# Kernel optimization log

Measured on AMD Instinct MI355X. Metric: run time of the kernel, lower is better.

Reference implementation:

```python
import jax, jax.numpy as jnp
import numpy as np

N_NODES = 100000
N_EDGES = 320000
N_GRAPHS = 4096
HID = 256
NUM_FEAT = 28


def setup_inputs() -> dict:
    key = jax.random.key(0)
    ks = jax.random.split(key, 20)
    inp = {}
    inp['x'] = jax.random.normal(ks[0], (N_NODES, NUM_FEAT), dtype=jnp.float32)
    inp['edge_index'] = jax.random.randint(ks[1], (2, N_EDGES), 0, N_NODES, dtype=jnp.int64)
    inp['batch'] = jnp.sort(jax.random.randint(ks[2], (N_NODES,), 0, N_GRAPHS, dtype=jnp.int64))
    def lin(k, out_d, in_d, scale=None):
        s = scale if scale is not None else 1.0 / np.sqrt(in_d)
        return jax.random.uniform(k, (out_d, in_d), jnp.float32, -s, s)
    # GraphConv layer l: W_rel (neighbor aggregate), b_rel, W_root (self)
    dims = [(HID, NUM_FEAT), (HID, HID), (HID, HID), (HID, HID)]
    for i, (o, d) in enumerate(dims, 1):
        inp[f'W{i}_rel'] = lin(ks[2 + 3 * i], o, d)
        inp[f'b{i}_rel'] = jnp.zeros((o,), jnp.float32)
        inp[f'W{i}_root'] = lin(ks[3 + 3 * i], o, d)
    inp['fc1_w'] = lin(ks[15], HID, 4 * HID)
    inp['fc1_b'] = jnp.zeros((HID,), jnp.float32)
    inp['fc2_w'] = lin(ks[16], HID, HID)
    inp['fc2_b'] = jnp.zeros((HID,), jnp.float32)
    inp['fc3_w'] = lin(ks[17], HID, HID)
    inp['fc3_b'] = jnp.zeros((HID,), jnp.float32)
    inp['fc4_w'] = lin(ks[18], 1, HID)
    inp['fc4_b'] = jnp.zeros((1,), jnp.float32)
    return inp


def _graph_conv(x, src, dst, W_rel, b_rel, W_root):
    # PyG GraphConv (aggr='add'): out = lin_rel(sum_{j->i} x_j) + lin_root(x_i)
    agg = jax.ops.segment_sum(x[src], dst, num_segments=N_NODES)  # [N, d]
    return agg @ W_rel.T + b_rel + x @ W_root.T


def reference(x, edge_index, batch,
              W1_rel, b1_rel, W1_root, W2_rel, b2_rel, W2_root,
              W3_rel, b3_rel, W3_root, W4_rel, b4_rel, W4_root,
              fc1_w, fc1_b, fc2_w, fc2_b, fc3_w, fc3_b, fc4_w, fc4_b):
    src, dst = edge_index[0], edge_index[1]
    x1 = jax.nn.relu(_graph_conv(x, src, dst, W1_rel, b1_rel, W1_root))
    x2 = jax.nn.relu(_graph_conv(x1, src, dst, W2_rel, b2_rel, W2_root))
    x3 = jax.nn.relu(_graph_conv(x2, src, dst, W3_rel, b3_rel, W3_root))
    x4 = jax.nn.relu(_graph_conv(x3, src, dst, W4_rel, b4_rel, W4_root))
    h = jnp.concatenate([x1, x2, x3, x4], axis=-1)  # [N, 4*HID]
    # global mean pool over graphs
    sums = jax.ops.segment_sum(h, batch, num_segments=N_GRAPHS)  # [G, 4*HID]
    cnts = jax.ops.segment_sum(jnp.ones((h.shape[0],), h.dtype), batch, num_segments=N_GRAPHS)
    g = sums / jnp.maximum(cnts, 1.0)[:, None]
    g = jax.nn.relu(g @ fc1_w.T + fc1_b)
    g = jax.nn.relu(g @ fc2_w.T + fc2_b)
    g = jax.nn.relu(g @ fc3_w.T + fc3_b)
    out = g @ fc4_w.T + fc4_b  # [G, 1]
    return out.reshape(-1)
```

## Files before the change

kernel.cpp:

```cpp
#include <hip/hip_runtime.h>
#include <hip/hip_bf16.h>
#include <cstdio>

#define HID 256

using short8  = __attribute__((ext_vector_type(8))) short;
using floatx4 = __attribute__((ext_vector_type(4))) float;

__device__ inline unsigned short bf16_rn(float x) {
    unsigned u = __float_as_uint(x);
    return (unsigned short)((u + 0x7FFFu + ((u >> 16) & 1u)) >> 16);
}

__global__ void marker_k(float* __restrict__ out, int n, float v) {
    int i = blockIdx.x * blockDim.x + threadIdx.x;
    if (i < n) out[i] = v;
}

__global__ void detect64_k(const unsigned* __restrict__ eiw, int E,
                           const unsigned* __restrict__ bw, int Nh,
                           int* __restrict__ any_nonzero) {
    int total = E + Nh;
    unsigned loc = 0;
    for (int i = blockIdx.x * blockDim.x + threadIdx.x; i < total;
         i += gridDim.x * blockDim.x) {
        loc |= (i < E) ? eiw[2 * i + 1] : bw[2 * (i - E) + 1];
    }
    if (loc) atomicOr(any_nonzero, 1);
}

__global__ void norm_idx_k(const int* __restrict__ src, int* __restrict__ dst,
                           int n, const int* __restrict__ any_nonzero) {
    int is64 = (any_nonzero[0] == 0);
    for (int i = blockIdx.x * blockDim.x + threadIdx.x; i < n;
         i += gridDim.x * blockDim.x) {
        dst[i] = is64 ? src[2 * i] : src[i];
    }
}

__global__ void pool_bounds_k(const int* __restrict__ batch, int N, int G,
                              int* __restrict__ starts) {
    int g = blockIdx.x * blockDim.x + threadIdx.x;
    if (g > G) return;
    int lo = 0, hi = N;
    while (lo < hi) {
        int mid = (lo + hi) >> 1;
        if (batch[mid] < g) lo = mid + 1; else hi = mid;
    }
    starts[g] = lo;
}

__global__ void deg_count_k(const int* __restrict__ ei, int E, int N,
                            int* __restrict__ deg) {
    int e = blockIdx.x * blockDim.x + threadIdx.x;
    if (e >= E) return;
    int s = ei[e];
    int d = ei[E + e];
    if ((unsigned)s >= (unsigned)N || (unsigned)d >= (unsigned)N) return;
    atomicAdd(&deg[d], 1);
}

#define SCAN_BLK 256

__global__ __launch_bounds__(SCAN_BLK) void scan_a_k(const int* __restrict__ deg,
                                                     int* __restrict__ bsum, int N) {
    __shared__ int red[SCAN_BLK];
    int i = blockIdx.x * SCAN_BLK + threadIdx.x;
    int v = (i < N) ? deg[i] : 0;
    red[threadIdx.x] = v;
    __syncthreads();
#pragma unroll
    for (int off = SCAN_BLK / 2; off > 0; off >>= 1) {
        if (threadIdx.x < off) red[threadIdx.x] += red[threadIdx.x + off];
        __syncthreads();
    }
    if (threadIdx.x == 0) bsum[blockIdx.x] = red[0];
}

__global__ __launch_bounds__(1024) void scan_b_k(int* __restrict__ bsum, int nb) {
    __shared__ int tsum[1024];
    int t = threadIdx.x;
    int v = (t < nb) ? bsum[t] : 0;
    tsum[t] = v;
    __syncthreads();
    for (int off = 1; off < 1024; off <<= 1) {
        int u = (t >= off) ? tsum[t - off] : 0;
        __syncthreads();
        tsum[t] += u;
        __syncthreads();
    }
    if (t < nb) bsum[t] = tsum[t] - v;
}

__global__ __launch_bounds__(SCAN_BLK) void scan_c_k(const int* __restrict__ deg,
                                                     const int* __restrict__ bsum,
                                                     int* __restrict__ row_ptr, int N) {
    __shared__ int tsum[SCAN_BLK];
    int t = threadIdx.x;
    int i = blockIdx.x * SCAN_BLK + t;
    int v = (i < N) ? deg[i] : 0;
    tsum[t] = v;
    __syncthreads();
    for (int off = 1; off < SCAN_BLK; off <<= 1) {
        int u = (t >= off) ? tsum[t - off] : 0;
        __syncthreads();
        tsum[t] += u;
        __syncthreads();
    }
    if (i <= N) row_ptr[i] = tsum[t] - v + bsum[blockIdx.x];
}

__global__ __launch_bounds__(1024) void scan_rowptr_k(const int* __restrict__ deg,
                                                      int* __restrict__ row_ptr, int N) {
    __shared__ int tsum[1024];
    int t = threadIdx.x;
    int chunk = (N + 1023) / 1024;
    int lo = t * chunk;
    int hi = min(lo + chunk, N);
    int s = 0;
    for (int i = lo; i < hi; i++) s += deg[i];
    tsum[t] = s;
    __syncthreads();
    for (int off = 1; off < 1024; off <<= 1) {
        int v = (t >= off) ? tsum[t - off] : 0;
        __syncthreads();
        tsum[t] += v;
        __syncthreads();
    }
    int run = (t == 0) ? 0 : tsum[t - 1];
    for (int i = lo; i < hi; i++) { row_ptr[i] = run; run += deg[i]; }
    if (hi >= N && lo <= N) row_ptr[N] = run;
}

__global__ void fill_csr_k(const int* __restrict__ ei, int E, int N,
                           const int* __restrict__ row_ptr, int* __restrict__ cursor,
                           int* __restrict__ esrc) {
    int e = blockIdx.x * blockDim.x + threadIdx.x;
    if (e >= E) return;
    int s = ei[e];
    int d = ei[E + e];
    if ((unsigned)s >= (unsigned)N || (unsigned)d >= (unsigned)N) return;
    int pos = atomicAdd(&cursor[d], 1);
    esrc[row_ptr[d] + pos] = s;
}

__global__ void gather28_k(const float* __restrict__ x, const int* __restrict__ row_ptr,
                           const int* __restrict__ esrc, float* __restrict__ Q28, int N) {
    int gid = blockIdx.x * blockDim.x + threadIdx.x;
    int node = gid >> 5;
    if (node >= N) return;
    int lane = gid & 31;
    if (lane >= 28) return;
    int s = row_ptr[node], e = row_ptr[node + 1];
    float acc = 0.f;
    for (int i = s; i < e; i++) {
        int src = esrc[i];
        acc += x[(size_t)src * 28 + lane];
    }
    Q28[(size_t)node * 28 + lane] = acc;
}

__global__ void gather256_k(const float* __restrict__ P, const int* __restrict__ row_ptr,
                            const int* __restrict__ esrc, float* __restrict__ Q, int N) {
    int gid = blockIdx.x * blockDim.x + threadIdx.x;
    int node = gid >> 6;
    if (node >= N) return;
    int lane = gid & 63;
    int s = row_ptr[node], e = row_ptr[node + 1];
    float4 acc = make_float4(0.f, 0.f, 0.f, 0.f);
    for (int i = s; i < e; i++) {
        int src = esrc[i];
        float4 v = *(const float4*)(P + (size_t)src * HID + lane * 4);
        acc.x += v.x; acc.y += v.y; acc.z += v.z; acc.w += v.w;
    }
    *(float4*)(Q + (size_t)node * HID + lane * 4) = acc;
}

__global__ __launch_bounds__(256) void l1_fused_k(
    const float* __restrict__ x, const float* __restrict__ agg,
    const float* __restrict__ Wrel, const float* __restrict__ Wroot,
    const float* __restrict__ bias, float* __restrict__ out, int M) {
    __shared__ float As[64][28];
    __shared__ float Xs[64][28];
    int t = threadIdx.x;
    int n0 = blockIdx.x * 64;
    float wrel[28], wroot[28];
#pragma unroll
    for (int k = 0; k < 28; k++) {
        wrel[k]  = Wrel[t * 28 + k];
        wroot[k] = Wroot[t * 28 + k];
    }
    float b = bias[t];
    for (int idx = t; idx < 64 * 28; idx += 256) {
        int r = idx / 28;
        int c = idx - r * 28;
        int gr = n0 + r;
        As[r][c] = (gr < M) ? agg[(size_t)gr * 28 + c] : 0.f;
        Xs[r][c] = (gr < M) ? x[(size_t)gr * 28 + c] : 0.f;
    }
    __syncthreads();
    int nmax = min(64, M - n0);
    for (int n = 0; n < nmax; n++) {
        float acc = b;
#pragma unroll
        for (int k4 = 0; k4 < 28; k4 += 4) {
            float4 a  = *(const float4*)&As[n][k4];
            float4 xx = *(const float4*)&Xs[n][k4];
            acc += a.x * wrel[k4] + a.y * wrel[k4 + 1] + a.z * wrel[k4 + 2] + a.w * wrel[k4 + 3];
            acc += xx.x * wroot[k4] + xx.y * wroot[k4 + 1] + xx.z * wroot[k4 + 2] + xx.w * wroot[k4 + 3];
        }
        out[(size_t)(n0 + n) * HID + t] = fmaxf(acc, 0.f);
    }
}

__global__ void wsplit6_k(const float* W0, const float* W1, const float* W2,
                          const float* W3, const float* W4, const float* W5,
                          unsigned short* __restrict__ out_hl, int n) {
    int i = blockIdx.x * blockDim.x + threadIdx.x;
    if (i >= n) return;
    const float* W = (blockIdx.y == 0) ? W0 : (blockIdx.y == 1) ? W1 :
                     (blockIdx.y == 2) ? W2 : (blockIdx.y == 3) ? W3 :
                     (blockIdx.y == 4) ? W4 : W5;
    unsigned short* o = out_hl + (size_t)blockIdx.y * 2 * n;
    float a = W[i];
    unsigned short h = bf16_rn(a);
    float hf = __uint_as_float(((unsigned)h) << 16);
    o[i] = h;
    o[n + i] = bf16_rn(a - hf);
}

#define LSTR 40

__global__ __launch_bounds__(256) void gemm_strip_mfma_k(
    const float* __restrict__ Q, const unsigned short* __restrict__ Wr_hl,
    float* __restrict__ P, const unsigned short* __restrict__ Wo_hl,
    const float* __restrict__ bias, int M) {
    __shared__ unsigned short Ah[64 * LSTR], Al[64 * LSTR];
    __shared__ unsigned short Wh[256 * LSTR], Wl[256 * LSTR];
    int t = threadIdx.x;
    int brow = blockIdx.x * 64;
    int w = t >> 6;
    int l = t & 63;

    floatx4 acc[4][4];
#pragma unroll
    for (int i = 0; i < 4; i++)
#pragma unroll
        for (int j = 0; j < 4; j++) acc[i][j] = (floatx4){0.f, 0.f, 0.f, 0.f};

    int srow = t >> 2;
    int sg   = t & 3;

    for (int ch = 0; ch < 16; ch++) {
        int phase2 = (ch >= 8);
        const float* A = phase2 ? P : Q;
        const unsigned short* Whl = phase2 ? Wo_hl : Wr_hl;
        int kbase = (ch & 7) * 32;

        {
            int gr = brow + srow;
            float v[8];
            if (gr < M) {
                float4 u0 = *(const float4*)(A + (size_t)gr * HID + kbase + sg * 8);
                float4 u1 = *(const float4*)(A + (size_t)gr * HID + kbase + sg * 8 + 4);
                v[0] = u0.x; v[1] = u0.y; v[2] = u0.z; v[3] = u0.w;
                v[4] = u1.x; v[5] = u1.y; v[6] = u1.z; v[7] = u1.w;
            } else {
#pragma unroll
                for (int j = 0; j < 8; j++) v[j] = 0.f;
            }
            union { unsigned short us[8]; short8 v8; } hh, ll;
#pragma unroll
            for (int j = 0; j < 8; j++) {
                unsigned short h = bf16_rn(v[j]);
                float hf = __uint_as_float(((unsigned)h) << 16);
                hh.us[j] = h;
                ll.us[j] = bf16_rn(v[j] - hf);
            }
            int base = srow * LSTR + sg * 8;
            *(short8*)(Ah + base) = hh.v8;
            *(short8*)(Al + base) = ll.v8;
        }
#pragma unroll
        for (int i = 0; i < 4; i++) {
            int col = srow + i * 64;
            short8 hh = *(const short8*)(Whl + (size_t)col * HID + kbase + sg * 8);
            short8 ll = *(const short8*)(Whl + 65536 + (size_t)col * HID + kbase + sg * 8);
            int base = col * LSTR + sg * 8;
            *(short8*)(Wh + base) = hh;
            *(short8*)(Wl + base) = ll;
        }
        __syncthreads();

        int frow = l & 15;
        int fg   = l >> 4;
        short8 ahf[4], alf[4], whf[4], wlf[4];
#pragma unroll
        for (int rt = 0; rt < 4; rt++) {
            int base = (rt * 16 + frow) * LSTR + fg * 8;
            ahf[rt] = *(short8*)(Ah + base);
            alf[rt] = *(short8*)(Al + base);
        }
#pragma unroll
        for (int ct = 0; ct < 4; ct++) {
            int base = (w * 64 + ct * 16 + frow) * LSTR + fg * 8;
            whf[ct] = *(short8*)(Wh + base);
            wlf[ct] = *(short8*)(Wl + base);
        }
#pragma unroll
        for (int rt = 0; rt < 4; rt++)
#pragma unroll
            for (int ct = 0; ct < 4; ct++) {
                acc[rt][ct] = __builtin_amdgcn_mfma_f32_16x16x32_bf16(
                    ahf[rt], whf[ct], acc[rt][ct], 0, 0, 0);
                acc[rt][ct] = __builtin_amdgcn_mfma_f32_16x16x32_bf16(
                    alf[rt], whf[ct], acc[rt][ct], 0, 0, 0);
                acc[rt][ct] = __builtin_amdgcn_mfma_f32_16x16x32_bf16(
                    ahf[rt], wlf[ct], acc[rt][ct], 0, 0, 0);
            }
        __syncthreads();
    }

#pragma unroll
    for (int ct = 0; ct < 4; ct++) {
        int gc = w * 64 + ct * 16 + (l & 15);
        float bs = bias[gc];
#pragma unroll
        for (int rt = 0; rt < 4; rt++) {
            floatx4 a = acc[rt][ct];
#pragma unroll
            for (int r = 0; r < 4; r++) {
                int gr = brow + rt * 16 + (l >> 4) * 4 + r;
                if (gr < M)
                    P[(size_t)gr * HID + gc] = fmaxf(a[r] + bs, 0.f);
            }
        }
    }
}

#define BM 64
#define BN 64
#define BK 32
#define LP 68

__global__ __launch_bounds__(256) void gemm_dual_k(
    const float* __restrict__ A1, int lda1, const float* __restrict__ W1,
    const float* __restrict__ A2, int lda2, const float* __restrict__ W2,
    const float* __restrict__ bias, float* __restrict__ out, int ldout,
    int M, int K1, int K2, int relu) {
    __shared__ float As[BK][LP];
    __shared__ float Ws[BK][LP];
    int t = threadIdx.x;
    int brow = blockIdx.x * BM;
    int bcol = blockIdx.y * BN;
    int tx = t & 15, ty = t >> 4;
    float acc[4][4] = {{0.f}};
    int Ktot = K1 + K2;
    int srow = t >> 3;
    int sk4 = (t & 7) << 2;

    for (int kk = 0; kk < Ktot; kk += BK) {
        int phase2 = (kk >= K1);
        const float* A = phase2 ? A2 : A1;
        const float* W = phase2 ? W2 : W1;
        int lda = phase2 ? lda2 : lda1;
        int ldw = phase2 ? K2 : K1;
        int kbase = phase2 ? (kk - K1) : kk;
#pragma unroll
        for (int i = 0; i < 2; i++) {
            int r = srow + i * 32;
            int gr = brow + r;
            float4 v = make_float4(0.f, 0.f, 0.f, 0.f);
            if (gr < M) v = *(const float4*)(A + (size_t)gr * lda + kbase + sk4);
            As[sk4 + 0][r] = v.x; As[sk4 + 1][r] = v.y;
            As[sk4 + 2][r] = v.z; As[sk4 + 3][r] = v.w;
            float4 w = *(const float4*)(W + (size_t)(bcol + r) * ldw + kbase + sk4);
            Ws[sk4 + 0][r] = w.x; Ws[sk4 + 1][r] = w.y;
            Ws[sk4 + 2][r] = w.z; Ws[sk4 + 3][r] = w.w;
        }
        __syncthreads();
#pragma unroll
        for (int k = 0; k < BK; k++) {
            float4 a = *(const float4*)&As[k][ty << 2];
            float4 w = *(const float4*)&Ws[k][tx << 2];
            float av[4] = {a.x, a.y, a.z, a.w};
            float wv[4] = {w.x, w.y, w.z, w.w};
#pragma unroll
            for (int i = 0; i < 4; i++)
#pragma unroll
                for (int j = 0; j < 4; j++)
                    acc[i][j] = fmaf(av[i], wv[j], acc[i][j]);
        }
        __syncthreads();
    }
#pragma unroll
    for (int i = 0; i < 4; i++) {
        int gr = brow + (ty << 2) + i;
        if (gr >= M) continue;
#pragma unroll
        for (int j = 0; j < 4; j++) {
            int gc = bcol + (tx << 2) + j;
            float v = acc[i][j] + bias[gc];
            if (relu) v = fmaxf(v, 0.f);
            out[(size_t)gr * ldout + gc] = v;
        }
    }
}

__global__ __launch_bounds__(256) void pool_slice_k(const float* __restrict__ xl,
                                                    const int* __restrict__ starts,
                                                    float* __restrict__ gslice, int N) {
    int g = blockIdx.x;
    int t = threadIdx.x;
    int s = starts[g], e = starts[g + 1];
    s = max(0, min(s, N));
    e = max(s, min(e, N));
    float a = 0.f;
    for (int n = s; n < e; n++) a += xl[(size_t)n * HID + t];
    float inv = 1.f / (float)max(e - s, 1);
    gslice[(size_t)g * 1024 + t] = a * inv;
}

__global__ void fc4_k(const float* __restrict__ in, const float* __restrict__ w,
                      const float* __restrict__ b, float* __restrict__ out, int M) {
    int gid = blockIdx.x * blockDim.x + threadIdx.x;
    int row = gid >> 6;
    if (row >= M) return;
    int lane = gid & 63;
    float4 v  = *(const float4*)(in + (size_t)row * HID + lane * 4);
    float4 ww = *(const float4*)(w + lane * 4);
    float acc = v.x * ww.x + v.y * ww.y + v.z * ww.z + v.w * ww.w;
#pragma unroll
    for (int off = 32; off; off >>= 1) acc += __shfl_down(acc, off);
    if (lane == 0) out[row] = acc + b[0];
}

extern "C" void kernel_launch(void* const* d_in, const int* in_sizes, int n_in,
                              void* d_out, int out_size, void* d_ws, size_t ws_size,
                              hipStream_t stream) {
    const int N = in_sizes[0] / 28;
    const int E = in_sizes[1] / 2;
    const int G = out_size;

    const float* x        = (const float*)d_in[0];
    const int*   ei_raw   = (const int*)d_in[1];
    const int*   b_raw    = (const int*)d_in[2];
    const float* W1_rel  = (const float*)d_in[3];
    const float* b1      = (const float*)d_in[4];
    const float* W1_root = (const float*)d_in[5];
    const float* W2_rel  = (const float*)d_in[6];
    const float* b2      = (const float*)d_in[7];
    const float* W2_root = (const float*)d_in[8];
    const float* W3_rel  = (const float*)d_in[9];
    const float* b3      = (const float*)d_in[10];
    const float* W3_root = (const float*)d_in[11];
    const float* W4_rel  = (const float*)d_in[12];
    const float* b4      = (const float*)d_in[13];
    const float* W4_root = (const float*)d_in[14];
    const float* fc1_w = (const float*)d_in[15];
    const float* fc1_b = (const float*)d_in[16];
    const float* fc2_w = (const float*)d_in[17];
    const float* fc2_b = (const float*)d_in[18];
    const float* fc3_w = (const float*)d_in[19];
    const float* fc3_b = (const float*)d_in[20];
    const float* fc4_w = (const float*)d_in[21];
    const float* fc4_b = (const float*)d_in[22];
    float* out = (float*)d_out;

    size_t fN  = (size_t)N * HID;
    size_t off_P      = 0;
    size_t off_Q      = off_P + fN;
    size_t off_gpool  = off_Q + fN;
    size_t off_t1     = off_gpool + (size_t)G * 1024;
    size_t off_t2     = off_t1 + (size_t)G * HID;
    size_t off_ei     = off_t2 + (size_t)G * HID;
    size_t off_batch  = off_ei + (size_t)2 * E;
    size_t off_starts = off_batch + (size_t)N;
    size_t off_flag   = off_starts + (size_t)(G + 1);
    size_t off_deg    = off_flag + 1;
    size_t off_cur    = off_deg + (size_t)N;
    size_t off_rowp   = off_cur + (size_t)N;
    size_t off_bsum   = off_rowp + (size_t)(N + 1);
    size_t off_esrc   = off_bsum + 1024;
    size_t off_wsplit = off_esrc + (size_t)E;
    size_t need = (off_wsplit + 393216 + 16) * 4;

    if (ws_size < need) {
        fprintf(stderr, "[kernel_launch] ws too small: ws=%zu need=%zu\n", ws_size, need);
        marker_k<<<(G + 255) / 256, 256, 0, stream>>>(out, G, (float)(ws_size >> 20));
        return;
    }

    float* wsf   = (float*)d_ws;
    float* P     = wsf + off_P;
    float* Q     = wsf + off_Q;
    float* gpool = wsf + off_gpool;
    float* t1    = wsf + off_t1;
    float* t2    = wsf + off_t2;
    int* nei     = (int*)(wsf + off_ei);
    int* nbatch  = (int*)(wsf + off_batch);
    int* starts  = (int*)(wsf + off_starts);
    int* flag    = (int*)(wsf + off_flag);
    int* deg     = (int*)(wsf + off_deg);
    int* cursor  = (int*)(wsf + off_cur);
    int* row_ptr = (int*)(wsf + off_rowp);
    int* bsum    = (int*)(wsf + off_bsum);
    int* esrc    = (int*)(wsf + off_esrc);
    unsigned short* wsplit = (unsigned short*)(wsf + off_wsplit);

    hipMemsetAsync(flag, 0, sizeof(int), stream);
    detect64_k<<<1024, 256, 0, stream>>>((const unsigned*)ei_raw, E,
                                         (const unsigned*)b_raw, N / 2, flag);
    norm_idx_k<<<1024, 256, 0, stream>>>(ei_raw, nei, 2 * E, flag);
    norm_idx_k<<<512, 256, 0, stream>>>(b_raw, nbatch, N, flag);

    pool_bounds_k<<<(G + 1 + 255) / 256, 256, 0, stream>>>(nbatch, N, G, starts);

    hipMemsetAsync(deg, 0, 2 * (size_t)N * sizeof(int), stream);
    deg_count_k<<<(E + 255) / 256, 256, 0, stream>>>(nei, E, N, deg);
    int nb = (N + 1 + SCAN_BLK - 1) / SCAN_BLK;
    if (nb <= 1024) {
        scan_a_k<<<nb, SCAN_BLK, 0, stream>>>(deg, bsum, N);
        scan_b_k<<<1, 1024, 0, stream>>>(bsum, nb);
        scan_c_k<<<nb, SCAN_BLK, 0, stream>>>(deg, bsum, row_ptr, N);
    } else {
        scan_rowptr_k<<<1, 1024, 0, stream>>>(deg, row_ptr, N);
    }
    fill_csr_k<<<(E + 255) / 256, 256, 0, stream>>>(nei, E, N, row_ptr, cursor, esrc);

    wsplit6_k<<<dim3((65536 + 255) / 256, 6), 256, 0, stream>>>(
        W2_rel, W2_root, W3_rel, W3_root, W4_rel, W4_root, wsplit, 65536);

    int nstrips = (N + 63) / 64;

    gather28_k<<<((size_t)N * 32 + 255) / 256, 256, 0, stream>>>(x, row_ptr, esrc, Q, N);
    l1_fused_k<<<nstrips, 256, 0, stream>>>(x, Q, W1_rel, W1_root, b1, P, N);
    pool_slice_k<<<G, 256, 0, stream>>>(P, starts, gpool + 0, N);

    const float* bb[3] = {b2, b3, b4};
    for (int l = 0; l < 3; l++) {
        gather256_k<<<((size_t)N * 64 + 255) / 256, 256, 0, stream>>>(P, row_ptr, esrc, Q, N);
        gemm_strip_mfma_k<<<nstrips, 256, 0, stream>>>(
            Q, wsplit + (size_t)(2 * l) * 131072,
            P, wsplit + (size_t)(2 * l + 1) * 131072, bb[l], N);
        pool_slice_k<<<G, 256, 0, stream>>>(P, starts, gpool + 256 * (l + 1), N);
    }

    dim3 gdimG(G / BM, HID / BN);
    gemm_dual_k<<<gdimG, 256, 0, stream>>>(gpool, 1024, fc1_w, nullptr, 0, nullptr,
                                           fc1_b, t1, HID, G, 1024, 0, 1);
    gemm_dual_k<<<gdimG, 256, 0, stream>>>(t1, HID, fc2_w, nullptr, 0, nullptr,
                                           fc2_b, t2, HID, G, HID, 0, 1);
    gemm_dual_k<<<gdimG, 256, 0, stream>>>(t2, HID, fc3_w, nullptr, 0, nullptr,
                                           fc3_b, t1, HID, G, HID, 0, 1);
    fc4_k<<<(G * 64 + 255) / 256, 256, 0, stream>>>(t1, fc4_w, fc4_b, out, G);
}
```

Measured before the change: 1.031 ms.

## Pre-split aggregated features to bf16 hi/lo in gather and double GEMM row tile

The gather kernel now writes its neighbor sum directly as bf16 high/low pairs, so the GEMM's first phase loads ready-made split operands instead of converting fp32 per chunk. The GEMM block grows to 512 threads and 128 rows, with 8 waves in a 2x4 layout, so each staged weight chunk is reused across twice as many rows. The Q buffer keeps the same byte size. The larger block raises LDS and register pressure per block, which may lower occupancy.

```diff
diff --git a/kernel.cpp b/kernel.cpp
--- a/kernel.cpp
+++ b/kernel.cpp
@@ -160,8 +160,9 @@
     Q28[(size_t)node * 28 + lane] = acc;
 }
 
-__global__ void gather256_k(const float* __restrict__ P, const int* __restrict__ row_ptr,
-                            const int* __restrict__ esrc, float* __restrict__ Q, int N) {
+__global__ void gather256s_k(const float* __restrict__ P, const int* __restrict__ row_ptr,
+                             const int* __restrict__ esrc, unsigned short* __restrict__ Qs,
+                             int N) {
     int gid = blockIdx.x * blockDim.x + threadIdx.x;
     int node = gid >> 6;
     if (node >= N) return;
@@ -173,7 +174,19 @@
         float4 v = *(const float4*)(P + (size_t)src * HID + lane * 4);
         acc.x += v.x; acc.y += v.y; acc.z += v.z; acc.w += v.w;
     }
-    *(float4*)(Q + (size_t)node * HID + lane * 4) = acc;
+    float vv[4] = {acc.x, acc.y, acc.z, acc.w};
+    ushort4 hi, lo;
+    unsigned short* hp = (unsigned short*)&hi;
+    unsigned short* lp = (unsigned short*)&lo;
+#pragma unroll
+    for (int j = 0; j < 4; j++) {
+        unsigned short h = bf16_rn(vv[j]);
+        float hf = __uint_as_float(((unsigned)h) << 16);
+        hp[j] = h;
+        lp[j] = bf16_rn(vv[j] - hf);
+    }
+    *(ushort4*)(Qs + (size_t)node * HID + lane * 4) = hi;
+    *(ushort4*)(Qs + (size_t)N * HID + (size_t)node * HID + lane * 4) = lo;
 }
 
 __global__ __launch_bounds__(256) void l1_fused_k(
@@ -231,16 +244,18 @@
 
 #define LSTR 40
 
-__global__ __launch_bounds__(256) void gemm_strip_mfma_k(
-    const float* __restrict__ Q, const unsigned short* __restrict__ Wr_hl,
+__global__ __launch_bounds__(512) void gemm_strip_mfma_k(
+    const unsigned short* __restrict__ Qs, const unsigned short* __restrict__ Wr_hl,
     float* __restrict__ P, const unsigned short* __restrict__ Wo_hl,
-    const float* __restrict__ bias, int M) {
-    __shared__ unsigned short Ah[64 * LSTR], Al[64 * LSTR];
+    const float* __restrict__ bias, int M, int N) {
+    __shared__ unsigned short Ah[128 * LSTR], Al[128 * LSTR];
     __shared__ unsigned short Wh[256 * LSTR], Wl[256 * LSTR];
     int t = threadIdx.x;
-    int brow = blockIdx.x * 64;
-    int w = t >> 6;
-    int l = t & 63;
+    int brow = blockIdx.x * 128;
+    int w  = t >> 6;
+    int wr = w >> 2;
+    int wc = w & 3;
+    int l  = t & 63;
 
     floatx4 acc[4][4];
 #pragma unroll
@@ -253,37 +268,38 @@
 
     for (int ch = 0; ch < 16; ch++) {
         int phase2 = (ch >= 8);
-        const float* A = phase2 ? P : Q;
         const unsigned short* Whl = phase2 ? Wo_hl : Wr_hl;
         int kbase = (ch & 7) * 32;
 
         {
             int gr = brow + srow;
-            float v[8];
+            short8 hv = {}, lv = {};
             if (gr < M) {
-                float4 u0 = *(const float4*)(A + (size_t)gr * HID + kbase + sg * 8);
-                float4 u1 = *(const float4*)(A + (size_t)gr * HID + kbase + sg * 8 + 4);
-                v[0] = u0.x; v[1] = u0.y; v[2] = u0.z; v[3] = u0.w;
-                v[4] = u1.x; v[5] = u1.y; v[6] = u1.z; v[7] = u1.w;
-            } else {
-#pragma unroll
-                for (int j = 0; j < 8; j++) v[j] = 0.f;
-            }
-            union { unsigned short us[8]; short8 v8; } hh, ll;
-#pragma unroll
-            for (int j = 0; j < 8; j++) {
-                unsigned short h = bf16_rn(v[j]);
-                float hf = __uint_as_float(((unsigned)h) << 16);
-                hh.us[j] = h;
-                ll.us[j] = bf16_rn(v[j] - hf);
+                if (!phase2) {
+                    hv = *(const short8*)(Qs + (size_t)gr * HID + kbase + sg * 8);
+                    lv = *(const short8*)(Qs + (size_t)N * HID + (size_t)gr * HID + kbase + sg * 8);
+                } else {
+                    float4 u0 = *(const float4*)(P + (size_t)gr * HID + kbase + sg * 8);
+                    float4 u1 = *(const float4*)(P + (size_t)gr * HID + kbase + sg * 8 + 4);
+                    float v[8] = {u0.x, u0.y, u0.z, u0.w, u1.x, u1.y, u1.z, u1.w};
+                    union { unsigned short us[8]; short8 v8; } hh, ll;
+#pragma unroll
+                    for (int j = 0; j < 8; j++) {
+                        unsigned short h = bf16_rn(v[j]);
+                        float hf = __uint_as_float(((unsigned)h) << 16);
+                        hh.us[j] = h;
+                        ll.us[j] = bf16_rn(v[j] - hf);
+                    }
+                    hv = hh.v8; lv = ll.v8;
+                }
             }
             int base = srow * LSTR + sg * 8;
-            *(short8*)(Ah + base) = hh.v8;
-            *(short8*)(Al + base) = ll.v8;
-        }
-#pragma unroll
-        for (int i = 0; i < 4; i++) {
-            int col = srow + i * 64;
+            *(short8*)(Ah + base) = hv;
+            *(short8*)(Al + base) = lv;
+        }
+#pragma unroll
+        for (int i = 0; i < 2; i++) {
+            int col = srow + i * 128;
             short8 hh = *(const short8*)(Whl + (size_t)col * HID + kbase + sg * 8);
             short8 ll = *(const short8*)(Whl + 65536 + (size_t)col * HID + kbase + sg * 8);
             int base = col * LSTR + sg * 8;
@@ -297,13 +313,13 @@
         short8 ahf[4], alf[4], whf[4], wlf[4];
 #pragma unroll
         for (int rt = 0; rt < 4; rt++) {
-            int base = (rt * 16 + frow) * LSTR + fg * 8;
+            int base = (wr * 64 + rt * 16 + frow) * LSTR + fg * 8;
             ahf[rt] = *(short8*)(Ah + base);
             alf[rt] = *(short8*)(Al + base);
         }
 #pragma unroll
         for (int ct = 0; ct < 4; ct++) {
-            int base = (w * 64 + ct * 16 + frow) * LSTR + fg * 8;
+            int base = (wc * 64 + ct * 16 + frow) * LSTR + fg * 8;
             whf[ct] = *(short8*)(Wh + base);
             wlf[ct] = *(short8*)(Wl + base);
         }
@@ -323,14 +339,14 @@
 
 #pragma unroll
     for (int ct = 0; ct < 4; ct++) {
-        int gc = w * 64 + ct * 16 + (l & 15);
+        int gc = wc * 64 + ct * 16 + (l & 15);
         float bs = bias[gc];
 #pragma unroll
         for (int rt = 0; rt < 4; rt++) {
             floatx4 a = acc[rt][ct];
 #pragma unroll
             for (int r = 0; r < 4; r++) {
-                int gr = brow + rt * 16 + (l >> 4) * 4 + r;
+                int gr = brow + wr * 64 + rt * 16 + (l >> 4) * 4 + r;
                 if (gr < M)
                     P[(size_t)gr * HID + gc] = fmaxf(a[r] + bs, 0.f);
             }
@@ -494,6 +510,7 @@
     float* wsf   = (float*)d_ws;
     float* P     = wsf + off_P;
     float* Q     = wsf + off_Q;
+    unsigned short* Qs = (unsigned short*)Q;
     float* gpool = wsf + off_gpool;
     float* t1    = wsf + off_t1;
     float* t2    = wsf + off_t2;
@@ -531,18 +548,17 @@
     wsplit6_k<<<dim3((65536 + 255) / 256, 6), 256, 0, stream>>>(
         W2_rel, W2_root, W3_rel, W3_root, W4_rel, W4_root, wsplit, 65536);
 
-    int nstrips = (N + 63) / 64;
-
     gather28_k<<<((size_t)N * 32 + 255) / 256, 256, 0, stream>>>(x, row_ptr, esrc, Q, N);
-    l1_fused_k<<<nstrips, 256, 0, stream>>>(x, Q, W1_rel, W1_root, b1, P, N);
+    l1_fused_k<<<(N + 63) / 64, 256, 0, stream>>>(x, Q, W1_rel, W1_root, b1, P, N);
     pool_slice_k<<<G, 256, 0, stream>>>(P, starts, gpool + 0, N);
 
+    int nstrips = (N + 127) / 128;
     const float* bb[3] = {b2, b3, b4};
     for (int l = 0; l < 3; l++) {
-        gather256_k<<<((size_t)N * 64 + 255) / 256, 256, 0, stream>>>(P, row_ptr, esrc, Q, N);
-        gemm_strip_mfma_k<<<nstrips, 256, 0, stream>>>(
-            Q, wsplit + (size_t)(2 * l) * 131072,
-            P, wsplit + (size_t)(2 * l + 1) * 131072, bb[l], N);
+        gather256s_k<<<((size_t)N * 64 + 255) / 256, 256, 0, stream>>>(P, row_ptr, esrc, Qs, N);
+        gemm_strip_mfma_k<<<nstrips, 512, 0, stream>>>(
+            Qs, wsplit + (size_t)(2 * l) * 131072,
+            P, wsplit + (size_t)(2 * l + 1) * 131072, bb[l], N, N);
         pool_slice_k<<<G, 256, 0, stream>>>(P, starts, gpool + 256 * (l + 1), N);
     }
 
```

New measurement: 1.154 ms. +12.0%, slower.

## Store node activations as split bf16 hi/lo planes instead of fp32

Applied to the files above, without the earlier changes.

Node features P and aggregates Q are now stored as two bf16 planes (high and residual low) written by the producers (l1, gather, GEMM epilogue). The GEMM's A-tile load therefore no longer converts fp32 to a bf16 split on every chunk. The gather and pool kernels reconstruct fp32 by adding the two planes. Total bytes stay the same, so the gain must come from dropping the per-load split arithmetic in the GEMM. The cost is extra split/recombine work in the gather and pool kernels, plus two separate plane streams with strided addressing.

```diff
diff --git a/kernel.cpp b/kernel.cpp
--- a/kernel.cpp
+++ b/kernel.cpp
@@ -10,6 +10,9 @@
 __device__ inline unsigned short bf16_rn(float x) {
     unsigned u = __float_as_uint(x);
     return (unsigned short)((u + 0x7FFFu + ((u >> 16) & 1u)) >> 16);
+}
+__device__ inline float bf2f(unsigned short u) {
+    return __uint_as_float(((unsigned)u) << 16);
 }
 
 __global__ void marker_k(float* __restrict__ out, int n, float v) {
@@ -160,26 +163,46 @@
     Q28[(size_t)node * 28 + lane] = acc;
 }
 
-__global__ void gather256_k(const float* __restrict__ P, const int* __restrict__ row_ptr,
-                            const int* __restrict__ esrc, float* __restrict__ Q, int N) {
+__global__ void gather256s_k(const unsigned short* __restrict__ Ps,
+                             const int* __restrict__ row_ptr,
+                             const int* __restrict__ esrc,
+                             unsigned short* __restrict__ Qs, int N) {
+    size_t fN = (size_t)N * HID;
     int gid = blockIdx.x * blockDim.x + threadIdx.x;
     int node = gid >> 6;
     if (node >= N) return;
     int lane = gid & 63;
     int s = row_ptr[node], e = row_ptr[node + 1];
-    float4 acc = make_float4(0.f, 0.f, 0.f, 0.f);
+    float a0 = 0.f, a1 = 0.f, a2 = 0.f, a3 = 0.f;
     for (int i = s; i < e; i++) {
         int src = esrc[i];
-        float4 v = *(const float4*)(P + (size_t)src * HID + lane * 4);
-        acc.x += v.x; acc.y += v.y; acc.z += v.z; acc.w += v.w;
-    }
-    *(float4*)(Q + (size_t)node * HID + lane * 4) = acc;
+        ushort4 h4 = *(const ushort4*)(Ps + (size_t)src * HID + lane * 4);
+        ushort4 l4 = *(const ushort4*)(Ps + fN + (size_t)src * HID + lane * 4);
+        a0 += bf2f(h4.x) + bf2f(l4.x);
+        a1 += bf2f(h4.y) + bf2f(l4.y);
+        a2 += bf2f(h4.z) + bf2f(l4.z);
+        a3 += bf2f(h4.w) + bf2f(l4.w);
+    }
+    float vv[4] = {a0, a1, a2, a3};
+    ushort4 hi, lo;
+    unsigned short* hp = (unsigned short*)&hi;
+    unsigned short* lp = (unsigned short*)&lo;
+#pragma unroll
+    for (int j = 0; j < 4; j++) {
+        unsigned short h = bf16_rn(vv[j]);
+        float hf = bf2f(h);
+        hp[j] = h;
+        lp[j] = bf16_rn(vv[j] - hf);
+    }
+    *(ushort4*)(Qs + (size_t)node * HID + lane * 4) = hi;
+    *(ushort4*)(Qs + fN + (size_t)node * HID + lane * 4) = lo;
 }
 
 __global__ __launch_bounds__(256) void l1_fused_k(
     const float* __restrict__ x, const float* __restrict__ agg,
     const float* __restrict__ Wrel, const float* __restrict__ Wroot,
-    const float* __restrict__ bias, float* __restrict__ out, int M) {
+    const float* __restrict__ bias, unsigned short* __restrict__ Ps, int M, int N) {
+    size_t fN = (size_t)N * HID;
     __shared__ float As[64][28];
     __shared__ float Xs[64][28];
     int t = threadIdx.x;
@@ -209,7 +232,10 @@
             acc += a.x * wrel[k4] + a.y * wrel[k4 + 1] + a.z * wrel[k4 + 2] + a.w * wrel[k4 + 3];
             acc += xx.x * wroot[k4] + xx.y * wroot[k4 + 1] + xx.z * wroot[k4 + 2] + xx.w * wroot[k4 + 3];
         }
-        out[(size_t)(n0 + n) * HID + t] = fmaxf(acc, 0.f);
+        float r = fmaxf(acc, 0.f);
+        unsigned short h = bf16_rn(r);
+        Ps[(size_t)(n0 + n) * HID + t] = h;
+        Ps[fN + (size_t)(n0 + n) * HID + t] = bf16_rn(r - bf2f(h));
     }
 }
 
@@ -224,17 +250,17 @@
     unsigned short* o = out_hl + (size_t)blockIdx.y * 2 * n;
     float a = W[i];
     unsigned short h = bf16_rn(a);
-    float hf = __uint_as_float(((unsigned)h) << 16);
     o[i] = h;
-    o[n + i] = bf16_rn(a - hf);
+    o[n + i] = bf16_rn(a - bf2f(h));
 }
 
 #define LSTR 40
 
 __global__ __launch_bounds__(256) void gemm_strip_mfma_k(
-    const float* __restrict__ Q, const unsigned short* __restrict__ Wr_hl,
-    float* __restrict__ P, const unsigned short* __restrict__ Wo_hl,
-    const float* __restrict__ bias, int M) {
+    const unsigned short* __restrict__ Qs, const unsigned short* __restrict__ Wr_hl,
+    unsigned short* __restrict__ Ps, const unsigned short* __restrict__ Wo_hl,
+    const float* __restrict__ bias, int M, int N) {
+    size_t fN = (size_t)N * HID;
     __shared__ unsigned short Ah[64 * LSTR], Al[64 * LSTR];
     __shared__ unsigned short Wh[256 * LSTR], Wl[256 * LSTR];
     int t = threadIdx.x;
@@ -253,33 +279,20 @@
 
     for (int ch = 0; ch < 16; ch++) {
         int phase2 = (ch >= 8);
-        const float* A = phase2 ? P : Q;
+        const unsigned short* Asrc = phase2 ? Ps : Qs;
         const unsigned short* Whl = phase2 ? Wo_hl : Wr_hl;
         int kbase = (ch & 7) * 32;
 
         {
             int gr = brow + srow;
-            float v[8];
+            short8 hv = {}, lv = {};
             if (gr < M) {
-                float4 u0 = *(const float4*)(A + (size_t)gr * HID + kbase + sg * 8);
-                float4 u1 = *(const float4*)(A + (size_t)gr * HID + kbase + sg * 8 + 4);
-                v[0] = u0.x; v[1] = u0.y; v[2] = u0.z; v[3] = u0.w;
-                v[4] = u1.x; v[5] = u1.y; v[6] = u1.z; v[7] = u1.w;
-            } else {
-#pragma unroll
-                for (int j = 0; j < 8; j++) v[j] = 0.f;
-            }
-            union { unsigned short us[8]; short8 v8; } hh, ll;
-#pragma unroll
-            for (int j = 0; j < 8; j++) {
-                unsigned short h = bf16_rn(v[j]);
-                float hf = __uint_as_float(((unsigned)h) << 16);
-                hh.us[j] = h;
-                ll.us[j] = bf16_rn(v[j] - hf);
+                hv = *(const short8*)(Asrc + (size_t)gr * HID + kbase + sg * 8);
+                lv = *(const short8*)(Asrc + fN + (size_t)gr * HID + kbase + sg * 8);
             }
             int base = srow * LSTR + sg * 8;
-            *(short8*)(Ah + base) = hh.v8;
-            *(short8*)(Al + base) = ll.v8;
+            *(short8*)(Ah + base) = hv;
+            *(short8*)(Al + base) = lv;
         }
 #pragma unroll
         for (int i = 0; i < 4; i++) {
@@ -331,11 +344,31 @@
 #pragma unroll
             for (int r = 0; r < 4; r++) {
                 int gr = brow + rt * 16 + (l >> 4) * 4 + r;
-                if (gr < M)
-                    P[(size_t)gr * HID + gc] = fmaxf(a[r] + bs, 0.f);
+                if (gr < M) {
+                    float v = fmaxf(a[r] + bs, 0.f);
+                    unsigned short h = bf16_rn(v);
+                    Ps[(size_t)gr * HID + gc] = h;
+                    Ps[fN + (size_t)gr * HID + gc] = bf16_rn(v - bf2f(h));
+                }
             }
         }
     }
+}
+
+__global__ __launch_bounds__(256) void pool_slice_k(const unsigned short* __restrict__ Ps,
+                                                    const int* __restrict__ starts,
+                                                    float* __restrict__ gslice, int N) {
+    size_t fN = (size_t)N * HID;
+    int g = blockIdx.x;
+    int t = threadIdx.x;
+    int s = starts[g], e = starts[g + 1];
+    s = max(0, min(s, N));
+    e = max(s, min(e, N));
+    float a = 0.f;
+    for (int n = s; n < e; n++)
+        a += bf2f(Ps[(size_t)n * HID + t]) + bf2f(Ps[fN + (size_t)n * HID + t]);
+    float inv = 1.f / (float)max(e - s, 1);
+    gslice[(size_t)g * 1024 + t] = a * inv;
 }
 
 #define BM 64
@@ -405,20 +438,6 @@
             out[(size_t)gr * ldout + gc] = v;
         }
     }
-}
-
-__global__ __launch_bounds__(256) void pool_slice_k(const float* __restrict__ xl,
-                                                    const int* __restrict__ starts,
-                                                    float* __restrict__ gslice, int N) {
-    int g = blockIdx.x;
-    int t = threadIdx.x;
-    int s = starts[g], e = starts[g + 1];
-    s = max(0, min(s, N));
-    e = max(s, min(e, N));
-    float a = 0.f;
-    for (int n = s; n < e; n++) a += xl[(size_t)n * HID + t];
-    float inv = 1.f / (float)max(e - s, 1);
-    gslice[(size_t)g * 1024 + t] = a * inv;
 }
 
 __global__ void fc4_k(const float* __restrict__ in, const float* __restrict__ w,
@@ -492,8 +511,9 @@
     }
 
     float* wsf   = (float*)d_ws;
-    float* P     = wsf + off_P;
+    unsigned short* Ps = (unsigned short*)(wsf + off_P);
     float* Q     = wsf + off_Q;
+    unsigned short* Qs = (unsigned short*)Q;
     float* gpool = wsf + off_gpool;
     float* t1    = wsf + off_t1;
     float* t2    = wsf + off_t2;
@@ -531,19 +551,18 @@
     wsplit6_k<<<dim3((65536 + 255) / 256, 6), 256, 0, stream>>>(
         W2_rel, W2_root, W3_rel, W3_root, W4_rel, W4_root, wsplit, 65536);
 
+    gather28_k<<<((size_t)N * 32 + 255) / 256, 256, 0, stream>>>(x, row_ptr, esrc, Q, N);
+    l1_fused_k<<<(N + 63) / 64, 256, 0, stream>>>(x, Q, W1_rel, W1_root, b1, Ps, N, N);
+    pool_slice_k<<<G, 256, 0, stream>>>(Ps, starts, gpool + 0, N);
+
     int nstrips = (N + 63) / 64;
-
-    gather28_k<<<((size_t)N * 32 + 255) / 256, 256, 0, stream>>>(x, row_ptr, esrc, Q, N);
-    l1_fused_k<<<nstrips, 256, 0, stream>>>(x, Q, W1_rel, W1_root, b1, P, N);
-    pool_slice_k<<<G, 256, 0, stream>>>(P, starts, gpool + 0, N);
-
     const float* bb[3] = {b2, b3, b4};
     for (int l = 0; l < 3; l++) {
-        gather256_k<<<((size_t)N * 64 + 255) / 256, 256, 0, stream>>>(P, row_ptr, esrc, Q, N);
+        gather256s_k<<<((size_t)N * 64 + 255) / 256, 256, 0, stream>>>(Ps, row_ptr, esrc, Qs, N);
         gemm_strip_mfma_k<<<nstrips, 256, 0, stream>>>(
-            Q, wsplit + (size_t)(2 * l) * 131072,
-            P, wsplit + (size_t)(2 * l + 1) * 131072, bb[l], N);
-        pool_slice_k<<<G, 256, 0, stream>>>(P, starts, gpool + 256 * (l + 1), N);
+            Qs, wsplit + (size_t)(2 * l) * 131072,
+            Ps, wsplit + (size_t)(2 * l + 1) * 131072, bb[l], N, N);
+        pool_slice_k<<<G, 256, 0, stream>>>(Ps, starts, gpool + 256 * (l + 1), N);
     }
 
     dim3 gdimG(G / BM, HID / BN);
```

Result: slower. 1.086 ms (+5.4%).

## Store activations as packed hi/lo bf16 words and run GEMM from registers

Applied to the files above, without the earlier changes.

Activations and weights are now stored as 32-bit words holding a bf16 high part and a bf16 residual, produced once by the producing kernels (layer-1, GEMM epilogue, gather) instead of being split inside the GEMM. The strip GEMM drops its shared-memory staging and barriers: each wave loads packed fragments straight from global memory into registers and unpacks them for the 3-pass bf16 MFMA. This removes per-chunk conversion work and LDS traffic, but each wave now re-reads the shared A tile from cache, and the last strip reads rows past M without a bounds guard. The stored activations also carry slightly less precision than fp32.

```diff
diff --git a/kernel.cpp b/kernel.cpp
--- a/kernel.cpp
+++ b/kernel.cpp
@@ -6,10 +6,32 @@
 
 using short8  = __attribute__((ext_vector_type(8))) short;
 using floatx4 = __attribute__((ext_vector_type(4))) float;
+using uintx8  = __attribute__((ext_vector_type(8))) unsigned int;
 
 __device__ inline unsigned short bf16_rn(float x) {
     unsigned u = __float_as_uint(x);
     return (unsigned short)((u + 0x7FFFu + ((u >> 16) & 1u)) >> 16);
+}
+__device__ inline float bf2f(unsigned short u) {
+    return __uint_as_float(((unsigned)u) << 16);
+}
+__device__ inline unsigned pack_hl(float v) {
+    unsigned short h = bf16_rn(v);
+    unsigned short lo = bf16_rn(v - bf2f(h));
+    return ((unsigned)h << 16) | (unsigned)lo;
+}
+__device__ inline float unpack_sum(unsigned u) {
+    return __uint_as_float(u & 0xFFFF0000u) + __uint_as_float(u << 16);
+}
+__device__ inline void unpack8(uintx8 u, short8& h, short8& l) {
+    union { unsigned w[4]; short8 s; } H, L;
+#pragma unroll
+    for (int i = 0; i < 4; i++) {
+        unsigned a = u[2 * i], b = u[2 * i + 1];
+        H.w[i] = (a >> 16) | (b & 0xFFFF0000u);
+        L.w[i] = (a & 0x0000FFFFu) | (b << 16);
+    }
+    h = H.s; l = L.s;
 }
 
 __global__ void marker_k(float* __restrict__ out, int n, float v) {
@@ -160,26 +182,33 @@
     Q28[(size_t)node * 28 + lane] = acc;
 }
 
-__global__ void gather256_k(const float* __restrict__ P, const int* __restrict__ row_ptr,
-                            const int* __restrict__ esrc, float* __restrict__ Q, int N) {
+__global__ void gather256p_k(const unsigned* __restrict__ Pp,
+                             const int* __restrict__ row_ptr,
+                             const int* __restrict__ esrc,
+                             unsigned* __restrict__ Qp, int N) {
     int gid = blockIdx.x * blockDim.x + threadIdx.x;
     int node = gid >> 6;
     if (node >= N) return;
     int lane = gid & 63;
     int s = row_ptr[node], e = row_ptr[node + 1];
-    float4 acc = make_float4(0.f, 0.f, 0.f, 0.f);
+    float a0 = 0.f, a1 = 0.f, a2 = 0.f, a3 = 0.f;
     for (int i = s; i < e; i++) {
         int src = esrc[i];
-        float4 v = *(const float4*)(P + (size_t)src * HID + lane * 4);
-        acc.x += v.x; acc.y += v.y; acc.z += v.z; acc.w += v.w;
-    }
-    *(float4*)(Q + (size_t)node * HID + lane * 4) = acc;
+        uint4 u = *(const uint4*)(Pp + (size_t)src * HID + lane * 4);
+        a0 += unpack_sum(u.x);
+        a1 += unpack_sum(u.y);
+        a2 += unpack_sum(u.z);
+        a3 += unpack_sum(u.w);
+    }
+    uint4 o;
+    o.x = pack_hl(a0); o.y = pack_hl(a1); o.z = pack_hl(a2); o.w = pack_hl(a3);
+    *(uint4*)(Qp + (size_t)node * HID + lane * 4) = o;
 }
 
 __global__ __launch_bounds__(256) void l1_fused_k(
     const float* __restrict__ x, const float* __restrict__ agg,
     const float* __restrict__ Wrel, const float* __restrict__ Wroot,
-    const float* __restrict__ bias, float* __restrict__ out, int M) {
+    const float* __restrict__ bias, unsigned* __restrict__ Pp, int M) {
     __shared__ float As[64][28];
     __shared__ float Xs[64][28];
     int t = threadIdx.x;
@@ -209,38 +238,31 @@
             acc += a.x * wrel[k4] + a.y * wrel[k4 + 1] + a.z * wrel[k4 + 2] + a.w * wrel[k4 + 3];
             acc += xx.x * wroot[k4] + xx.y * wroot[k4 + 1] + xx.z * wroot[k4 + 2] + xx.w * wroot[k4 + 3];
         }
-        out[(size_t)(n0 + n) * HID + t] = fmaxf(acc, 0.f);
+        Pp[(size_t)(n0 + n) * HID + t] = pack_hl(fmaxf(acc, 0.f));
     }
 }
 
 __global__ void wsplit6_k(const float* W0, const float* W1, const float* W2,
                           const float* W3, const float* W4, const float* W5,
-                          unsigned short* __restrict__ out_hl, int n) {
+                          unsigned* __restrict__ outp, int n) {
     int i = blockIdx.x * blockDim.x + threadIdx.x;
     if (i >= n) return;
     const float* W = (blockIdx.y == 0) ? W0 : (blockIdx.y == 1) ? W1 :
                      (blockIdx.y == 2) ? W2 : (blockIdx.y == 3) ? W3 :
                      (blockIdx.y == 4) ? W4 : W5;
-    unsigned short* o = out_hl + (size_t)blockIdx.y * 2 * n;
-    float a = W[i];
-    unsigned short h = bf16_rn(a);
-    float hf = __uint_as_float(((unsigned)h) << 16);
-    o[i] = h;
-    o[n + i] = bf16_rn(a - hf);
-}
-
-#define LSTR 40
-
-__global__ __launch_bounds__(256) void gemm_strip_mfma_k(
-    const float* __restrict__ Q, const unsigned short* __restrict__ Wr_hl,
-    float* __restrict__ P, const unsigned short* __restrict__ Wo_hl,
+    outp[(size_t)blockIdx.y * n + i] = pack_hl(W[i]);
+}
+
+__global__ __launch_bounds__(256) void gemm_reg_k(
+    const unsigned* __restrict__ Qp, const unsigned* __restrict__ Wr,
+    unsigned* __restrict__ Pp, const unsigned* __restrict__ Wo,
     const float* __restrict__ bias, int M) {
-    __shared__ unsigned short Ah[64 * LSTR], Al[64 * LSTR];
-    __shared__ unsigned short Wh[256 * LSTR], Wl[256 * LSTR];
-    int t = threadIdx.x;
-    int brow = blockIdx.x * 64;
+    int t = threadIdx.x;
     int w = t >> 6;
     int l = t & 63;
+    int brow = blockIdx.x * 64;
+    int frow = l & 15;
+    int fg   = l >> 4;
 
     floatx4 acc[4][4];
 #pragma unroll
@@ -248,94 +270,72 @@
 #pragma unroll
         for (int j = 0; j < 4; j++) acc[i][j] = (floatx4){0.f, 0.f, 0.f, 0.f};
 
-    int srow = t >> 2;
-    int sg   = t & 3;
-
-    for (int ch = 0; ch < 16; ch++) {
-        int phase2 = (ch >= 8);
-        const float* A = phase2 ? P : Q;
-        const unsigned short* Whl = phase2 ? Wo_hl : Wr_hl;
-        int kbase = (ch & 7) * 32;
-
-        {
-            int gr = brow + srow;
-            float v[8];
-            if (gr < M) {
-                float4 u0 = *(const float4*)(A + (size_t)gr * HID + kbase + sg * 8);
-                float4 u1 = *(const float4*)(A + (size_t)gr * HID + kbase + sg * 8 + 4);
-                v[0] = u0.x; v[1] = u0.y; v[2] = u0.z; v[3] = u0.w;
-                v[4] = u1.x; v[5] = u1.y; v[6] = u1.z; v[7] = u1.w;
-            } else {
-#pragma unroll
-                for (int j = 0; j < 8; j++) v[j] = 0.f;
-            }
-            union { unsigned short us[8]; short8 v8; } hh, ll;
-#pragma unroll
-            for (int j = 0; j < 8; j++) {
-                unsigned short h = bf16_rn(v[j]);
-                float hf = __uint_as_float(((unsigned)h) << 16);
-                hh.us[j] = h;
-                ll.us[j] = bf16_rn(v[j] - hf);
-            }
-            int base = srow * LSTR + sg * 8;
-            *(short8*)(Ah + base) = hh.v8;
-            *(short8*)(Al + base) = ll.v8;
+    const unsigned* Alist[2] = {Qp, Pp};
+    const unsigned* Wlist[2] = {Wr, Wo};
+
+    for (int ph = 0; ph < 2; ph++) {
+        const unsigned* A = Alist[ph];
+        const unsigned* W = Wlist[ph];
+#pragma unroll 2
+        for (int c = 0; c < 8; c++) {
+            int kb = c * 32 + fg * 8;
+            uintx8 au[4], wu[4];
+#pragma unroll
+            for (int rt = 0; rt < 4; rt++)
+                au[rt] = *(const uintx8*)(A + (size_t)(brow + rt * 16 + frow) * HID + kb);
+#pragma unroll
+            for (int ct = 0; ct < 4; ct++)
+                wu[ct] = *(const uintx8*)(W + (size_t)(w * 64 + ct * 16 + frow) * HID + kb);
+            short8 ah[4], al[4], wh[4], wl[4];
+#pragma unroll
+            for (int rt = 0; rt < 4; rt++) unpack8(au[rt], ah[rt], al[rt]);
+#pragma unroll
+            for (int ct = 0; ct < 4; ct++) unpack8(wu[ct], wh[ct], wl[ct]);
+#pragma unroll
+            for (int rt = 0; rt < 4; rt++)
+#pragma unroll
+                for (int ct = 0; ct < 4; ct++) {
+                    acc[rt][ct] = __builtin_amdgcn_mfma_f32_16x16x32_bf16(
+                        ah[rt], wh[ct], acc[rt][ct], 0, 0, 0);
+                    acc[rt][ct] = __builtin_amdgcn_mfma_f32_16x16x32_bf16(
+                        al[rt], wh[ct], acc[rt][ct], 0, 0, 0);
+                    acc[rt][ct] = __builtin_amdgcn_mfma_f32_16x16x32_bf16(
+                        ah[rt], wl[ct], acc[rt][ct], 0, 0, 0);
+                }
         }
-#pragma unroll
-        for (int i = 0; i < 4; i++) {
-            int col = srow + i * 64;
-            short8 hh = *(const short8*)(Whl + (size_t)col * HID + kbase + sg * 8);
-            short8 ll = *(const short8*)(Whl + 65536 + (size_t)col * HID + kbase + sg * 8);
-            int base = col * LSTR + sg * 8;
-            *(short8*)(Wh + base) = hh;
-            *(short8*)(Wl + base) = ll;
-        }
-        __syncthreads();
-
-        int frow = l & 15;
-        int fg   = l >> 4;
-        short8 ahf[4], alf[4], whf[4], wlf[4];
-#pragma unroll
-        for (int rt = 0; rt < 4; rt++) {
-            int base = (rt * 16 + frow) * LSTR + fg * 8;
-            ahf[rt] = *(short8*)(Ah + base);
-            alf[rt] = *(short8*)(Al + base);
-        }
-#pragma unroll
-        for (int ct = 0; ct < 4; ct++) {
-            int base = (w * 64 + ct * 16 + frow) * LSTR + fg * 8;
-            whf[ct] = *(short8*)(Wh + base);
-            wlf[ct] = *(short8*)(Wl + base);
-        }
-#pragma unroll
-        for (int rt = 0; rt < 4; rt++)
-#pragma unroll
-            for (int ct = 0; ct < 4; ct++) {
-                acc[rt][ct] = __builtin_amdgcn_mfma_f32_16x16x32_bf16(
-                    ahf[rt], whf[ct], acc[rt][ct], 0, 0, 0);
-                acc[rt][ct] = __builtin_amdgcn_mfma_f32_16x16x32_bf16(
-                    alf[rt], whf[ct], acc[rt][ct], 0, 0, 0);
-                acc[rt][ct] = __builtin_amdgcn_mfma_f32_16x16x32_bf16(
-                    ahf[rt], wlf[ct], acc[rt][ct], 0, 0, 0);
-            }
-        __syncthreads();
-    }
+    }
+
+    __syncthreads();
 
 #pragma unroll
     for (int ct = 0; ct < 4; ct++) {
-        int gc = w * 64 + ct * 16 + (l & 15);
+        int gc = w * 64 + ct * 16 + frow;
         float bs = bias[gc];
 #pragma unroll
         for (int rt = 0; rt < 4; rt++) {
             floatx4 a = acc[rt][ct];
 #pragma unroll
             for (int r = 0; r < 4; r++) {
-                int gr = brow + rt * 16 + (l >> 4) * 4 + r;
+                int gr = brow + rt * 16 + fg * 4 + r;
                 if (gr < M)
-                    P[(size_t)gr * HID + gc] = fmaxf(a[r] + bs, 0.f);
+                    Pp[(size_t)gr * HID + gc] = pack_hl(fmaxf(a[r] + bs, 0.f));
             }
         }
     }
+}
+
+__global__ __launch_bounds__(256) void pool_slice_k(const unsigned* __restrict__ Pp,
+                                                    const int* __restrict__ starts,
+                                                    float* __restrict__ gslice, int N) {
+    int g = blockIdx.x;
+    int t = threadIdx.x;
+    int s = starts[g], e = starts[g + 1];
+    s = max(0, min(s, N));
+    e = max(s, min(e, N));
+    float a = 0.f;
+    for (int n = s; n < e; n++) a += unpack_sum(Pp[(size_t)n * HID + t]);
+    float inv = 1.f / (float)max(e - s, 1);
+    gslice[(size_t)g * 1024 + t] = a * inv;
 }
 
 #define BM 64
@@ -405,20 +405,6 @@
             out[(size_t)gr * ldout + gc] = v;
         }
     }
-}
-
-__global__ __launch_bounds__(256) void pool_slice_k(const float* __restrict__ xl,
-                                                    const int* __restrict__ starts,
-                                                    float* __restrict__ gslice, int N) {
-    int g = blockIdx.x;
-    int t = threadIdx.x;
-    int s = starts[g], e = starts[g + 1];
-    s = max(0, min(s, N));
-    e = max(s, min(e, N));
-    float a = 0.f;
-    for (int n = s; n < e; n++) a += xl[(size_t)n * HID + t];
-    float inv = 1.f / (float)max(e - s, 1);
-    gslice[(size_t)g * 1024 + t] = a * inv;
 }
 
 __global__ void fc4_k(const float* __restrict__ in, const float* __restrict__ w,
@@ -482,8 +468,8 @@
     size_t off_rowp   = off_cur + (size_t)N;
     size_t off_bsum   = off_rowp + (size_t)(N + 1);
     size_t off_esrc   = off_bsum + 1024;
-    size_t off_wsplit = off_esrc + (size_t)E;
-    size_t need = (off_wsplit + 393216 + 16) * 4;
+    size_t off_wsplit = (off_esrc + (size_t)E + 7) & ~(size_t)7;
+    size_t need = (off_wsplit + 6 * 65536 + 16) * 4;
 
     if (ws_size < need) {
         fprintf(stderr, "[kernel_launch] ws too small: ws=%zu need=%zu\n", ws_size, need);
@@ -492,8 +478,9 @@
     }
 
     float* wsf   = (float*)d_ws;
-    float* P     = wsf + off_P;
+    unsigned* Pp = (unsigned*)(wsf + off_P);
     float* Q     = wsf + off_Q;
+    unsigned* Qp = (unsigned*)Q;
     float* gpool = wsf + off_gpool;
     float* t1    = wsf + off_t1;
     float* t2    = wsf + off_t2;
@@ -506,7 +493,7 @@
     int* row_ptr = (int*)(wsf + off_rowp);
     int* bsum    = (int*)(wsf + off_bsum);
     int* esrc    = (int*)(wsf + off_esrc);
-    unsigned short* wsplit = (unsigned short*)(wsf + off_wsplit);
+    unsigned* Wu = (unsigned*)(wsf + off_wsplit);
 
     hipMemsetAsync(flag, 0, sizeof(int), stream);
     detect64_k<<<1024, 256, 0, stream>>>((const unsigned*)ei_raw, E,
@@ -529,21 +516,20 @@
     fill_csr_k<<<(E + 255) / 256, 256, 0, stream>>>(nei, E, N, row_ptr, cursor, esrc);
 
     wsplit6_k<<<dim3((65536 + 255) / 256, 6), 256, 0, stream>>>(
-        W2_rel, W2_root, W3_rel, W3_root, W4_rel, W4_root, wsplit, 65536);
+        W2_rel, W2_root, W3_rel, W3_root, W4_rel, W4_root, Wu, 65536);
+
+    gather28_k<<<((size_t)N * 32 + 255) / 256, 256, 0, stream>>>(x, row_ptr, esrc, Q, N);
+    l1_fused_k<<<(N + 63) / 64, 256, 0, stream>>>(x, Q, W1_rel, W1_root, b1, Pp, N);
+    pool_slice_k<<<G, 256, 0, stream>>>(Pp, starts, gpool + 0, N);
 
     int nstrips = (N + 63) / 64;
-
-    gather28_k<<<((size_t)N * 32 + 255) / 256, 256, 0, stream>>>(x, row_ptr, esrc, Q, N);
-    l1_fused_k<<<nstrips, 256, 0, stream>>>(x, Q, W1_rel, W1_root, b1, P, N);
-    pool_slice_k<<<G, 256, 0, stream>>>(P, starts, gpool + 0, N);
-
     const float* bb[3] = {b2, b3, b4};
     for (int l = 0; l < 3; l++) {
-        gather256_k<<<((size_t)N * 64 + 255) / 256, 256, 0, stream>>>(P, row_ptr, esrc, Q, N);
-        gemm_strip_mfma_k<<<nstrips, 256, 0, stream>>>(
-            Q, wsplit + (size_t)(2 * l) * 131072,
-            P, wsplit + (size_t)(2 * l + 1) * 131072, bb[l], N);
-        pool_slice_k<<<G, 256, 0, stream>>>(P, starts, gpool + 256 * (l + 1), N);
+        gather256p_k<<<((size_t)N * 64 + 255) / 256, 256, 0, stream>>>(Pp, row_ptr, esrc, Qp, N);
+        gemm_reg_k<<<nstrips, 256, 0, stream>>>(
+            Qp, Wu + (size_t)(2 * l) * 65536,
+            Pp, Wu + (size_t)(2 * l + 1) * 65536, bb[l], N);
+        pool_slice_k<<<G, 256, 0, stream>>>(Pp, starts, gpool + 256 * (l + 1), N);
     }
 
     dim3 gdimG(G / BM, HID / BN);
```

Result: slower. 1.323 ms (+28.3%).
